# Kernel tuning notes

Hardware: AMD Instinct MI355X
Metric: run time of the kernel (lower is better)

Reference implementation:

```python
import jax, jax.numpy as jnp
import numpy as np

HIDDEN = 768
NUM_HEADS = 12
HEAD_DIM = HIDDEN // NUM_HEADS  # 64


def setup_inputs() -> dict:
    key = jax.random.key(0)
    ks = jax.random.split(key, 7)
    B, S = 2, 4096
    scale = 1.0 / np.sqrt(HIDDEN)
    return {
        "hidden_states": jax.random.normal(ks[0], (B, S, HIDDEN), dtype=jnp.float32),
        "Wq": jax.random.normal(ks[1], (HIDDEN, HIDDEN), dtype=jnp.float32) * scale,
        "bq": jnp.zeros((HIDDEN,), dtype=jnp.float32),
        "Wk": jax.random.normal(ks[2], (HIDDEN, HIDDEN), dtype=jnp.float32) * scale,
        "bk": jnp.zeros((HIDDEN,), dtype=jnp.float32),
        "Wv": jax.random.normal(ks[3], (HIDDEN, HIDDEN), dtype=jnp.float32) * scale,
        "bv": jnp.zeros((HIDDEN,), dtype=jnp.float32),
    }


def _split_heads(x):
    # [B, S, H] -> [B, heads, S, head_dim]
    B, S, _ = x.shape
    return x.reshape(B, S, NUM_HEADS, HEAD_DIM).transpose(0, 2, 1, 3)


def reference(hidden_states, Wq, bq, Wk, bk, Wv, bv):
    q = _split_heads(hidden_states @ Wq + bq)  # [B, h, S, d]
    k = _split_heads(hidden_states @ Wk + bk)
    v = _split_heads(hidden_states @ Wv + bv)
    scores = jnp.einsum("bhqd,bhkd->bhqk", q, k) / np.sqrt(HEAD_DIM)
    probs = jax.nn.softmax(scores, axis=-1)  # [B, h, S, S] materialized (eager attn)
    ctx = jnp.einsum("bhqk,bhkd->bhqd", probs, v)
    B, _, S, _ = ctx.shape
    return ctx.transpose(0, 2, 1, 3).reshape(B, S, HIDDEN)
```

## Files before the change

### kernel.cpp

```cpp
#include <hip/hip_runtime.h>
#include <hip/hip_bf16.h>

typedef unsigned short ushort_t;
typedef __attribute__((ext_vector_type(4))) float f32x4;
typedef __attribute__((ext_vector_type(8))) __bf16 bfrag;

#define MFMA16(a,b,c) __builtin_amdgcn_mfma_f32_16x16x32_bf16((a),(b),(c),0,0,0)

#define HID 768
#define NH 12
#define SEQ 4096
#define QSCALE 0.18033688011112042f

#define DRAIN_VMEM() asm volatile("s_waitcnt vmcnt(0)" ::: "memory")

__device__ __forceinline__ unsigned short f2bf(float x) {
  union { float f; unsigned u; } v; v.f = x;
  unsigned r = v.u + 0x7fffu + ((v.u >> 16) & 1u);
  return (unsigned short)(r >> 16);
}

typedef const unsigned char __attribute__((address_space(1)))* gas1_t;
typedef unsigned char __attribute__((address_space(3)))* las3_t;
__device__ __forceinline__ void gload_lds16(const void* g, void* l) {
  __builtin_amdgcn_global_load_lds((gas1_t)(unsigned long long)g,
                                   (las3_t)(unsigned)(unsigned long long)l,
                                   16, 0, 0);
}

__device__ __forceinline__ f32x4 zero4() { f32x4 z = {0.f, 0.f, 0.f, 0.f}; return z; }

__global__ __launch_bounds__(256) void cvt_hidden(const float* __restrict__ hs,
                                                  ushort_t* __restrict__ A) {
  int i = blockIdx.x * 256 + threadIdx.x;
  float4 v = ((const float4*)hs)[i];
  ushort4 o;
  o.x = f2bf(v.x); o.y = f2bf(v.y); o.z = f2bf(v.z); o.w = f2bf(v.w);
  ((ushort4*)A)[i] = o;
}

__global__ __launch_bounds__(256) void transpose_w(const float* __restrict__ Wq,
                                                   const float* __restrict__ Wk,
                                                   const float* __restrict__ Wv,
                                                   ushort_t* __restrict__ Wt) {
  const int z = blockIdx.z;
  const float* W = (z == 0) ? Wq : ((z == 1) ? Wk : Wv);
  const int k0 = blockIdx.x * 64, n0 = blockIdx.y * 64;
  __shared__ float tile[64][65];
  const int t = threadIdx.x;
  const int c4 = (t & 15) * 4;
  const int r = t >> 4;
#pragma unroll
  for (int it = 0; it < 4; ++it) {
    int rr = r + it * 16;
    float4 v = *(const float4*)&W[(size_t)(k0 + rr) * HID + n0 + c4];
    tile[c4 + 0][rr] = v.x; tile[c4 + 1][rr] = v.y;
    tile[c4 + 2][rr] = v.z; tile[c4 + 3][rr] = v.w;
  }
  __syncthreads();
#pragma unroll
  for (int it = 0; it < 4; ++it) {
    int nl = r + it * 16;
    ushort4 o;
    o.x = f2bf(tile[nl][c4 + 0]); o.y = f2bf(tile[nl][c4 + 1]);
    o.z = f2bf(tile[nl][c4 + 2]); o.w = f2bf(tile[nl][c4 + 3]);
    *(ushort4*)&Wt[((size_t)z * HID + n0 + nl) * HID + k0 + c4] = o;
  }
}

__global__ __launch_bounds__(256) void qkv_gemm(const ushort_t* __restrict__ A,
                                                const ushort_t* __restrict__ Wt,
                                                const float* __restrict__ bq,
                                                const float* __restrict__ bk,
                                                const float* __restrict__ bv,
                                                ushort_t* __restrict__ Qh,
                                                ushort_t* __restrict__ Kh,
                                                ushort_t* __restrict__ Vt) {
  __shared__ ushort_t Als[128 * 64];
  __shared__ ushort_t Bls[128 * 64];
  const int z = blockIdx.z;
  const int m0 = blockIdx.x * 128, n0 = blockIdx.y * 128;
  const ushort_t* Wz = Wt + (size_t)z * HID * HID;
  const float* bias = (z == 0) ? bq : ((z == 1) ? bk : bv);
  const int t = threadIdx.x, w = t >> 6, lane = t & 63;
  const int g = lane >> 4, qc = lane & 15;
  const int srow = lane >> 3, sch = lane & 7;
  const int wm = w >> 1, wn = w & 1;

  f32x4 acc[4][4];
#pragma unroll
  for (int mt = 0; mt < 4; ++mt)
#pragma unroll
    for (int nt = 0; nt < 4; ++nt) acc[mt][nt] = zero4();

  for (int kt = 0; kt < 12; ++kt) {
    const int k0 = kt * 64;
#pragma unroll
    for (int i = 0; i < 4; ++i) {
      int row = w * 32 + i * 8 + srow;
      int chA = sch ^ (srow & 7);
      gload_lds16(&A[(size_t)(m0 + row) * HID + k0 + chA * 8],
                  &Als[(w * 32 + i * 8) * 64]);
      gload_lds16(&Wz[(size_t)(n0 + row) * HID + k0 + chA * 8],
                  &Bls[(w * 32 + i * 8) * 64]);
    }
    DRAIN_VMEM();
    __syncthreads();
#pragma unroll
    for (int kk = 0; kk < 2; ++kk) {
      bfrag af[4], bf_[4];
#pragma unroll
      for (int mt = 0; mt < 4; ++mt) {
        int row = wm * 64 + mt * 16 + qc;
        af[mt] = *(const bfrag*)((const char*)Als + row * 128 +
                                 (((kk * 4 + g) ^ (qc & 7)) << 4));
      }
#pragma unroll
      for (int nt = 0; nt < 4; ++nt) {
        int row = wn * 64 + nt * 16 + qc;
        bf_[nt] = *(const bfrag*)((const char*)Bls + row * 128 +
                                  (((kk * 4 + g) ^ (qc & 7)) << 4));
      }
#pragma unroll
      for (int mt = 0; mt < 4; ++mt)
#pragma unroll
        for (int nt = 0; nt < 4; ++nt)
          acc[mt][nt] = MFMA16(af[mt], bf_[nt], acc[mt][nt]);
    }
    __syncthreads();
  }

#pragma unroll
  for (int mt = 0; mt < 4; ++mt) {
#pragma unroll
    for (int nt = 0; nt < 4; ++nt) {
      int n = n0 + wn * 64 + nt * 16 + qc;
      int head = n >> 6, d = n & 63;
      float bb = bias[n];
      int mB = m0 + wm * 64 + mt * 16 + 4 * g;
      int bidx = mB >> 12, s0 = mB & 4095;
      f32x4 a = acc[mt][nt];
      if (z == 2) {
        ushort4 o;
        o.x = f2bf(a[0] + bb); o.y = f2bf(a[1] + bb);
        o.z = f2bf(a[2] + bb); o.w = f2bf(a[3] + bb);
        int scol = (s0 & ~31) | (((s0 >> 2) & 3) << 3) | (((s0 >> 4) & 1) << 2);
        *(ushort4*)&Vt[((size_t)((bidx * NH + head) * 64 + d)) * SEQ + scol] = o;
      } else {
        ushort_t* dst = (z == 0) ? Qh : Kh;
        float sc = (z == 0) ? QSCALE : 1.0f;
        size_t base = (size_t)(bidx * NH + head) * SEQ;
#pragma unroll
        for (int i = 0; i < 4; ++i)
          dst[(base + s0 + i) * 64 + d] = f2bf((a[i] + bb) * sc);
      }
    }
  }
}

__global__ __launch_bounds__(256, 3) void attn_kernel(const ushort_t* __restrict__ Qh,
                                                      const ushort_t* __restrict__ Kh,
                                                      const ushort_t* __restrict__ Vt,
                                                      float* __restrict__ out) {
  const int bh = blockIdx.y;
  const int b = bh / NH, head = bh - b * NH;
  const int t = threadIdx.x, w = t >> 6, lane = t & 63;
  const int g = lane >> 4, qc = lane & 15;
  const int qh = w >> 1, kh = w & 1;
  const ushort_t* Qb = Qh + (size_t)bh * SEQ * 64;
  const ushort_t* Kb = Kh + (size_t)bh * SEQ * 64;
  const ushort_t* Vb = Vt + (size_t)bh * 64 * SEQ;
  const int q0 = blockIdx.x * 64 + qh * 32;

  __shared__ ushort_t Kls[2][4096];
  __shared__ ushort_t Vls[2][4096];

  int jr[2], jc[2];
#pragma unroll
  for (int i = 0; i < 2; ++i) {
    int j = w * 128 + i * 64 + lane;
    jr[i] = j >> 3;
    jc[i] = (j & 7) ^ (jr[i] & 7);
  }

  bfrag qv[2][2];
#pragma unroll
  for (int qf = 0; qf < 2; ++qf)
#pragma unroll
    for (int dd = 0; dd < 2; ++dd)
      qv[qf][dd] = *(const bfrag*)&Qb[(size_t)(q0 + qf * 16 + qc) * 64 + dd * 32 + g * 8];

  f32x4 o[2][4];
  f32x4 lacc[2];
#pragma unroll
  for (int qf = 0; qf < 2; ++qf) {
    lacc[qf] = zero4();
#pragma unroll
    for (int dt = 0; dt < 4; ++dt) o[qf][dt] = zero4();
  }
  bfrag ones;
#pragma unroll
  for (int j = 0; j < 8; ++j) ones[j] = (__bf16)1.0f;

#pragma unroll
  for (int i = 0; i < 2; ++i) {
    gload_lds16(&Kb[(size_t)jr[i] * 64 + jc[i] * 8], &Kls[0][(w * 128 + i * 64) * 8]);
    gload_lds16(&Vb[(size_t)jr[i] * SEQ + jc[i] * 8], &Vls[0][(w * 128 + i * 64) * 8]);
  }

  for (int kt = 0; kt < 64; ++kt) {
    const int cur = kt & 1;
    DRAIN_VMEM();
    __syncthreads();
    if (kt < 63) {
      const int kbn = (kt + 1) * 64;
#pragma unroll
      for (int i = 0; i < 2; ++i) {
        gload_lds16(&Kb[(size_t)(kbn + jr[i]) * 64 + jc[i] * 8],
                    &Kls[cur ^ 1][(w * 128 + i * 64) * 8]);
        gload_lds16(&Vb[(size_t)jr[i] * SEQ + kbn + jc[i] * 8],
                    &Vls[cur ^ 1][(w * 128 + i * 64) * 8]);
      }
    }
    const ushort_t* Kc = Kls[cur];
    const ushort_t* Vc = Vls[cur];

    bfrag ak[2][2];
#pragma unroll
    for (int s = 0; s < 2; ++s) {
      const int r = kh * 32 + s * 16 + qc;
      ak[s][0] = *(const bfrag*)&Kc[r * 64 + ((g ^ (qc & 7)) * 8)];
      ak[s][1] = *(const bfrag*)&Kc[r * 64 + (((4 + g) ^ (qc & 7)) * 8)];
    }
    bfrag av[4];
#pragma unroll
    for (int dt = 0; dt < 4; ++dt)
      av[dt] = *(const bfrag*)&Vc[(dt * 16 + qc) * 64 + (((kh * 4 + g) ^ (qc & 7)) * 8)];

    bfrag bpq[2];
#pragma unroll
    for (int qf = 0; qf < 2; ++qf) {
      f32x4 st[2];
#pragma unroll
      for (int s = 0; s < 2; ++s) {
        f32x4 zz = zero4();
        zz = MFMA16(ak[s][0], qv[qf][0], zz);
        st[s] = MFMA16(ak[s][1], qv[qf][1], zz);
      }
      bfrag p;
#pragma unroll
      for (int i = 0; i < 4; ++i) {
        p[i]     = (__bf16)__builtin_amdgcn_exp2f(st[0][i]);
        p[4 + i] = (__bf16)__builtin_amdgcn_exp2f(st[1][i]);
      }
      bpq[qf] = p;
      lacc[qf] = MFMA16(ones, p, lacc[qf]);
    }

#pragma unroll
    for (int dt = 0; dt < 4; ++dt) {
      o[0][dt] = MFMA16(av[dt], bpq[0], o[0][dt]);
      o[1][dt] = MFMA16(av[dt], bpq[1], o[1][dt]);
    }
  }

  __syncthreads();
  float* redO = (float*)&Kls[0][0];
  float* redL = (float*)&Vls[0][0];
  if (kh == 1) {
#pragma unroll
    for (int qf = 0; qf < 2; ++qf) {
#pragma unroll
      for (int dt = 0; dt < 4; ++dt)
        *(f32x4*)&redO[qh * 2048 + (qf * 4 + dt) * 256 + lane * 4] = o[qf][dt];
      redL[qh * 128 + qf * 64 + lane] = lacc[qf][0];
    }
  }
  __syncthreads();
  if (kh == 0) {
#pragma unroll
    for (int qf = 0; qf < 2; ++qf) {
      float l = lacc[qf][0] + redL[qh * 128 + qf * 64 + lane];
      float inv = 1.0f / l;
      int qrow = q0 + qf * 16 + qc;
      float* orow = out + (size_t)(b * SEQ + qrow) * HID + head * 64;
#pragma unroll
      for (int dt = 0; dt < 4; ++dt) {
        f32x4 p = *(f32x4*)&redO[qh * 2048 + (qf * 4 + dt) * 256 + lane * 4];
        f32x4 s = o[qf][dt] + p;
        float4 vv;
        vv.x = s[0] * inv; vv.y = s[1] * inv; vv.z = s[2] * inv; vv.w = s[3] * inv;
        *(float4*)(orow + dt * 16 + 4 * g) = vv;
      }
    }
  }
}

extern "C" void kernel_launch(void* const* d_in, const int* in_sizes, int n_in,
                              void* d_out, int out_size, void* d_ws, size_t ws_size,
                              hipStream_t stream) {
  (void)in_sizes; (void)n_in; (void)out_size; (void)ws_size;
  const float* hs = (const float*)d_in[0];
  const float* Wq = (const float*)d_in[1];
  const float* bq = (const float*)d_in[2];
  const float* Wk = (const float*)d_in[3];
  const float* bk = (const float*)d_in[4];
  const float* Wv = (const float*)d_in[5];
  const float* bv = (const float*)d_in[6];
  float* out = (float*)d_out;

  char* ws = (char*)d_ws;
  ushort_t* Abf = (ushort_t*)ws;
  ushort_t* Wt  = (ushort_t*)(ws + 12582912);
  ushort_t* Qh  = (ushort_t*)(ws + 12582912 + 3538944);
  ushort_t* Kh  = Qh + 6291456;
  ushort_t* Vt  = Kh + 6291456;

  cvt_hidden<<<6144, 256, 0, stream>>>(hs, Abf);
  transpose_w<<<dim3(12, 12, 3), 256, 0, stream>>>(Wq, Wk, Wv, Wt);
  qkv_gemm<<<dim3(64, 6, 3), 256, 0, stream>>>(Abf, Wt, bq, bk, bv, Qh, Kh, Vt);
  attn_kernel<<<dim3(64, 24), 256, 0, stream>>>(Qh, Kh, Vt, out);
}
```

Measured before the change: 174.4 us.

## Double attention block to 512 threads sharing K/V tiles, add MFMA priority hints

The attention kernel now runs 8 waves per block covering 128 query rows instead of 64, so each K/V tile staged in LDS is reused by twice as many queries and global K/V traffic per query halves. Each thread issues one async load per tile instead of two. The reduction scratch is split across the K and V buffers, with a separate redL array. s_setprio hints are wrapped around the MFMA sections to favour matrix issue. The trade-offs are half as many blocks (768) for the GPU to distribute, a larger per-block barrier cost, and a tighter register budget under launch_bounds(512,4).

Measured after the change: 164.5 us. 1.06x faster.

```diff
diff --git a/kernel.cpp b/kernel.cpp
--- a/kernel.cpp
+++ b/kernel.cpp
@@ -158,7 +158,7 @@
   }
 }
 
-__global__ __launch_bounds__(256, 3) void attn_kernel(const ushort_t* __restrict__ Qh,
+__global__ __launch_bounds__(512, 4) void attn_kernel(const ushort_t* __restrict__ Qh,
                                                       const ushort_t* __restrict__ Kh,
                                                       const ushort_t* __restrict__ Vt,
                                                       float* __restrict__ out) {
@@ -170,18 +170,14 @@
   const ushort_t* Qb = Qh + (size_t)bh * SEQ * 64;
   const ushort_t* Kb = Kh + (size_t)bh * SEQ * 64;
   const ushort_t* Vb = Vt + (size_t)bh * 64 * SEQ;
-  const int q0 = blockIdx.x * 64 + qh * 32;
+  const int q0 = blockIdx.x * 128 + qh * 32;
 
   __shared__ ushort_t Kls[2][4096];
   __shared__ ushort_t Vls[2][4096];
-
-  int jr[2], jc[2];
-#pragma unroll
-  for (int i = 0; i < 2; ++i) {
-    int j = w * 128 + i * 64 + lane;
-    jr[i] = j >> 3;
-    jc[i] = (j & 7) ^ (jr[i] & 7);
-  }
+  __shared__ float    redL[512];
+
+  const int jr = t >> 3;
+  const int jc = (t & 7) ^ (jr & 7);
 
   bfrag qv[2][2];
 #pragma unroll
@@ -202,11 +198,8 @@
 #pragma unroll
   for (int j = 0; j < 8; ++j) ones[j] = (__bf16)1.0f;
 
-#pragma unroll
-  for (int i = 0; i < 2; ++i) {
-    gload_lds16(&Kb[(size_t)jr[i] * 64 + jc[i] * 8], &Kls[0][(w * 128 + i * 64) * 8]);
-    gload_lds16(&Vb[(size_t)jr[i] * SEQ + jc[i] * 8], &Vls[0][(w * 128 + i * 64) * 8]);
-  }
+  gload_lds16(&Kb[(size_t)jr * 64 + jc * 8], &Kls[0][w * 512]);
+  gload_lds16(&Vb[(size_t)jr * SEQ + jc * 8], &Vls[0][w * 512]);
 
   for (int kt = 0; kt < 64; ++kt) {
     const int cur = kt & 1;
@@ -214,13 +207,8 @@
     __syncthreads();
     if (kt < 63) {
       const int kbn = (kt + 1) * 64;
-#pragma unroll
-      for (int i = 0; i < 2; ++i) {
-        gload_lds16(&Kb[(size_t)(kbn + jr[i]) * 64 + jc[i] * 8],
-                    &Kls[cur ^ 1][(w * 128 + i * 64) * 8]);
-        gload_lds16(&Vb[(size_t)jr[i] * SEQ + kbn + jc[i] * 8],
-                    &Vls[cur ^ 1][(w * 128 + i * 64) * 8]);
-      }
+      gload_lds16(&Kb[(size_t)(kbn + jr) * 64 + jc * 8], &Kls[cur ^ 1][w * 512]);
+      gload_lds16(&Vb[(size_t)jr * SEQ + kbn + jc * 8], &Vls[cur ^ 1][w * 512]);
     }
     const ushort_t* Kc = Kls[cur];
     const ushort_t* Vc = Vls[cur];
@@ -241,12 +229,14 @@
 #pragma unroll
     for (int qf = 0; qf < 2; ++qf) {
       f32x4 st[2];
+      __builtin_amdgcn_s_setprio(1);
 #pragma unroll
       for (int s = 0; s < 2; ++s) {
         f32x4 zz = zero4();
         zz = MFMA16(ak[s][0], qv[qf][0], zz);
         st[s] = MFMA16(ak[s][1], qv[qf][1], zz);
       }
+      __builtin_amdgcn_s_setprio(0);
       bfrag p;
 #pragma unroll
       for (int i = 0; i < 4; ++i) {
@@ -257,22 +247,26 @@
       lacc[qf] = MFMA16(ones, p, lacc[qf]);
     }
 
+    __builtin_amdgcn_s_setprio(1);
 #pragma unroll
     for (int dt = 0; dt < 4; ++dt) {
       o[0][dt] = MFMA16(av[dt], bpq[0], o[0][dt]);
       o[1][dt] = MFMA16(av[dt], bpq[1], o[1][dt]);
     }
+    __builtin_amdgcn_s_setprio(0);
   }
 
   __syncthreads();
-  float* redO = (float*)&Kls[0][0];
-  float* redL = (float*)&Vls[0][0];
+  float* redK = (float*)&Kls[0][0];
+  float* redV = (float*)&Vls[0][0];
+  float* redO = (qh < 2) ? redK : redV;
+  const int ro = (((qh & 1) * 2) * 4) * 256;
   if (kh == 1) {
 #pragma unroll
     for (int qf = 0; qf < 2; ++qf) {
 #pragma unroll
       for (int dt = 0; dt < 4; ++dt)
-        *(f32x4*)&redO[qh * 2048 + (qf * 4 + dt) * 256 + lane * 4] = o[qf][dt];
+        *(f32x4*)&redO[ro + (qf * 4 + dt) * 256 + lane * 4] = o[qf][dt];
       redL[qh * 128 + qf * 64 + lane] = lacc[qf][0];
     }
   }
@@ -286,7 +280,7 @@
       float* orow = out + (size_t)(b * SEQ + qrow) * HID + head * 64;
 #pragma unroll
       for (int dt = 0; dt < 4; ++dt) {
-        f32x4 p = *(f32x4*)&redO[qh * 2048 + (qf * 4 + dt) * 256 + lane * 4];
+        f32x4 p = *(f32x4*)&redO[ro + (qf * 4 + dt) * 256 + lane * 4];
         f32x4 s = o[qf][dt] + p;
         float4 vv;
         vv.x = s[0] * inv; vv.y = s[1] * inv; vv.z = s[2] * inv; vv.w = s[3] * inv;
@@ -319,5 +313,5 @@
   cvt_hidden<<<6144, 256, 0, stream>>>(hs, Abf);
   transpose_w<<<dim3(12, 12, 3), 256, 0, stream>>>(Wq, Wk, Wv, Wt);
   qkv_gemm<<<dim3(64, 6, 3), 256, 0, stream>>>(Abf, Wt, bq, bk, bv, Qh, Kh, Vt);
-  attn_kernel<<<dim3(64, 24), 256, 0, stream>>>(Qh, Kh, Vt, out);
-}
+  attn_kernel<<<dim3(32, 24), 512, 0, stream>>>(Qh, Kh, Vt, out);
+}
```
